# Performance work log

Hardware: AMD Instinct MI355X
Metric: run time of the kernel (lower is better)

The kernel has to match this reference:

```python
import jax, jax.numpy as jnp
import numpy as np

V, D, L, H, HD, S = 50257, 768, 8, 6, 128, 2048
BS = 128          # flex-attention BLOCK_SIZE
EOS = 50256       # document separator token
EPS = 1.1920929e-07  # torch F.rms_norm default eps (f32 machine eps)
ATTN_SCALE = 0.12


def rms(x):
    return x * jax.lax.rsqrt(jnp.mean(jnp.square(x), axis=-1, keepdims=True) + EPS)


def rope_tables(seq_len, hd):
    # modded-nanogpt rotary: hd//4 geometric freqs + hd//4 zero freqs, applied to half-split dims
    freqs = (1.0 / 1024.0) ** jnp.linspace(0.0, 1.0, hd // 4)
    freqs = jnp.concatenate([freqs, jnp.zeros(hd // 4, dtype=jnp.float32)])
    theta = jnp.arange(seq_len, dtype=jnp.float32)[:, None] * freqs[None, :]  # [S, hd//2]
    return jnp.cos(theta), jnp.sin(theta)


def rope(x, cos, sin):  # x: [B,S,H,hd]
    x1, x2 = jnp.split(x, 2, axis=-1)
    c = cos[None, :, None, :]
    s = sin[None, :, None, :]
    return jnp.concatenate([x1 * c + x2 * s, -x1 * s + x2 * c], axis=-1)


def build_token_mask(input_seq, w):
    # Reproduces BlockMask.from_kv_blocks semantics: per query-row keep the w-1 most
    # recent FULL blocks and min(n_partial, max(w - n_full, 1)) most recent PARTIAL
    # blocks; mask_mod (document-causal) applies inside partial blocks only.
    NB = S // BS
    docs = jnp.cumsum((input_seq == EOS).astype(jnp.int32))
    bi = jnp.arange(NB)
    dr = docs.reshape(NB, BS)
    dl, dh = dr[:, 0], dr[:, -1]
    m_any = (bi[:, None] >= bi[None, :]) & (dl[:, None] <= dh[None, :]) & (dh[:, None] >= dl[None, :])
    m_all = (bi[:, None] > bi[None, :]) & (dl[:, None] == dh[None, :]) & (dh[:, None] == dl[None, :])
    part = m_any & ~m_all
    nf = m_all.sum(-1)

    def keep_most_recent(m, kcount):  # keep kcount True entries with largest kv index
        r = jnp.cumsum(m[:, ::-1].astype(jnp.int32), axis=-1)[:, ::-1]
        return m & (r <= kcount[:, None])

    kf = keep_most_recent(m_all, jnp.minimum(nf, w - 1))
    kp = keep_most_recent(part, jnp.minimum(part.sum(-1), jnp.maximum(w - nf, 1)))
    tf = jnp.repeat(jnp.repeat(kf, BS, 0), BS, 1)   # [S,S]
    tp = jnp.repeat(jnp.repeat(kp, BS, 0), BS, 1)
    q = jnp.arange(S)
    tok = (q[:, None] >= q[None, :]) & (docs[:, None] == docs[None, :])
    return tf | (tp & tok)


def _forward(input_seq, sliding_window_num_blocks, target_seq, embed, ve_embeds,
             qkv_w, attn_proj_w, mlp_fc_w, mlp_proj_w, scalars):
    cos, sin = rope_tables(S, HD)
    long_m = build_token_mask(input_seq, sliding_window_num_blocks)
    short_m = build_token_mask(input_seq, sliding_window_num_blocks // 2)
    cycle = [long_m, short_m, short_m, short_m]
    masks = (cycle * ((L + 3) // 4))[:L - 1] + [long_m]

    ve_tok = ve_embeds[:, input_seq, :]  # [3,S,D]
    ve = [ve_tok[0], ve_tok[1], ve_tok[2]] + [None] * (L - 6) + [ve_tok[0], ve_tok[1], ve_tok[2]]

    skip_w = scalars[:L]
    lambdas = scalars[L:3 * L].reshape(L, 2)
    sa_lambdas = scalars[3 * L:5 * L].reshape(L, 2)

    stride = max(1, L // 4)
    skip_map = {}
    for m in range(3):
        i = L - 3 + m
        j = i - stride * (m + 1)
        if 0 <= j < i < L:
            skip_map[i] = j

    x = x0 = rms(embed[input_seq])[None]  # [1,S,D]
    skips = []
    for i in range(L):
        if i in skip_map:
            x = x + skip_w[skip_map[i]] * skips[skip_map[i]]
        lam, sal = lambdas[i], sa_lambdas[i]
        # Block: residual mix with x0, attn, mlp (modded-nanogpt style)
        x = lam[0] * x + lam[1] * x0
        xa = rms(x)
        qkv = (xa @ qkv_w[i].T).reshape(1, S, 3 * H, HD)
        q, k, v = jnp.split(qkv, 3, axis=2)
        q = rope(rms(q), cos, sin)
        k = rope(rms(k), cos, sin)
        if ve[i] is not None:
            v = sal[0] * v + sal[1] * ve[i].reshape(1, S, H, HD)
        else:
            v = sal[0] * v
        scores = jnp.einsum('bqhd,bkhd->bhqk', q, k) * ATTN_SCALE
        scores = jnp.where(masks[i][None, None], scores, -jnp.inf)
        y = jnp.einsum('bhqk,bkhd->bqhd', jax.nn.softmax(scores, axis=-1), v)
        x = x + y.reshape(1, S, H * HD) @ attn_proj_w[i].T
        h = jnp.square(jax.nn.relu(rms(x) @ mlp_fc_w[i].T))
        x = x + h @ mlp_proj_w[i].T
        skips.append(x)

    x = rms(x)
    logits = (x[0].astype(jnp.bfloat16) @ embed.T.astype(jnp.bfloat16)).astype(jnp.float32)
    cap = 15.0 * logits * jax.lax.rsqrt(jnp.square(logits) + 225.0)  # softcap
    lsm = jax.nn.log_softmax(cap, axis=-1)
    return -jnp.mean(lsm[jnp.arange(S), target_seq])


def setup_inputs() -> dict:
    key = jax.random.key(0)
    ks = jax.random.split(key, 9)
    input_seq = jax.random.randint(ks[0], (S,), 0, V)
    input_seq = input_seq.at[jnp.arange(0, S, 512)].set(EOS)  # inject doc boundaries
    target_seq = jax.random.randint(ks[1], (S,), 0, V)
    embed = jax.random.normal(ks[2], (V, D), jnp.float32)
    ve_embeds = jax.random.normal(ks[3], (3, V, D), jnp.float32)
    sd = 1.0 / np.sqrt(D)
    qkv_w = jax.random.normal(ks[4], (L, 3 * H * HD, D), jnp.float32) * sd
    attn_proj_w = jax.random.normal(ks[5], (L, D, H * HD), jnp.float32) * (1.0 / np.sqrt(H * HD))
    mlp_fc_w = jax.random.normal(ks[6], (L, 4 * D, D), jnp.float32) * sd
    mlp_proj_w = jax.random.normal(ks[7], (L, D, 4 * D), jnp.float32) * (1.0 / np.sqrt(4 * D))
    scalars = jnp.concatenate([
        jnp.ones(L), jnp.tile(jnp.array([1.0, 0.0]), L), jnp.tile(jnp.array([0.5, 0.5]), L)
    ]).astype(jnp.float32) + 0.02 * jax.random.normal(ks[8], (5 * L,), jnp.float32)
    return {"input_seq": input_seq, "sliding_window_num_blocks": 8, "target_seq": target_seq,
            "embed": embed, "ve_embeds": ve_embeds, "qkv_w": qkv_w, "attn_proj_w": attn_proj_w,
            "mlp_fc_w": mlp_fc_w, "mlp_proj_w": mlp_proj_w, "scalars": scalars}


def reference(input_seq, sliding_window_num_blocks, target_seq, embed, ve_embeds,
              qkv_w, attn_proj_w, mlp_fc_w, mlp_proj_w, scalars):
    return _forward(input_seq, sliding_window_num_blocks, target_seq, embed, ve_embeds,
                    qkv_w, attn_proj_w, mlp_fc_w, mlp_proj_w, scalars)
```

## Files before the change

### kernel.cpp

```cpp
#include <hip/hip_runtime.h>
#include <hip/hip_bf16.h>
#include <math.h>

#define NSEQ 2048
#define NDIM 768
#define NLAY 8
#define NHEAD 6
#define NHD 128
#define NVOC 50257
#define NBLK 16
#define BLKSZ 128
#define EOS_TOK 50256
#define EPSF 1.1920929e-07f
#define ASCALE 0.12f
#define NVT 393
#define CAPSH 15.f

#define GSWZ(r) (((r) ^ ((r) >> 2)) & 3)

using bf16x8 = __attribute__((ext_vector_type(8))) __bf16;
using bf16x4 = __attribute__((ext_vector_type(4))) __bf16;
using f32x4  = __attribute__((ext_vector_type(4))) float;

__device__ __forceinline__ __bf16 tobf(float x) {
  __hip_bfloat16 h = __float2bfloat16(x);
  return *reinterpret_cast<__bf16*>(&h);
}

__global__ __launch_bounds__(256) void cvt_bf16_kernel(const float* __restrict__ in, __bf16* __restrict__ out,
                                                       long n) {
  long i = ((long)blockIdx.x * blockDim.x + threadIdx.x) * 4;
  long stride = (long)gridDim.x * blockDim.x * 4;
  for (; i < n; i += stride) {
    float4 v = *(const float4*)(in + i);
    bf16x4 o;
    o[0] = tobf(v.x); o[1] = tobf(v.y); o[2] = tobf(v.z); o[3] = tobf(v.w);
    *(bf16x4*)(out + i) = o;
  }
}

__global__ __launch_bounds__(1024) void prep_kernel(const int* __restrict__ seq, const int* __restrict__ wptr,
                                                    int* __restrict__ docs, int* __restrict__ catL,
                                                    int* __restrict__ catS) {
  __shared__ int f[NSEQ];
  __shared__ int g[NSEQ];
  int tid = threadIdx.x;
  for (int i = tid; i < NSEQ; i += 1024) f[i] = (seq[i] == EOS_TOK) ? 1 : 0;
  __syncthreads();
  int* a = f; int* b = g;
  for (int off = 1; off < NSEQ; off <<= 1) {
    for (int i = tid; i < NSEQ; i += 1024) {
      int v = a[i];
      if (i >= off) v += a[i - off];
      b[i] = v;
    }
    __syncthreads();
    int* t = a; a = b; b = t;
  }
  for (int i = tid; i < NSEQ; i += 1024) docs[i] = a[i];
  __syncthreads();
  if (tid == 0) {
    int dl[NBLK], dh[NBLK];
    for (int bi = 0; bi < NBLK; ++bi) { dl[bi] = a[bi * BLKSZ]; dh[bi] = a[bi * BLKSZ + BLKSZ - 1]; }
    int W = *wptr;
    for (int pass = 0; pass < 2; ++pass) {
      int w = (pass == 0) ? W : (W / 2);
      int* cat = (pass == 0) ? catL : catS;
      for (int i = 0; i < NBLK; ++i) {
        int allr[NBLK], partr[NBLK];
        int nf = 0, np = 0;
        for (int j = 0; j < NBLK; ++j) {
          int any_ = (i >= j) && (dl[i] <= dh[j]) && (dh[i] >= dl[j]);
          int all_ = (i > j) && (dl[i] == dh[j]) && (dh[i] == dl[j]);
          allr[j] = all_; partr[j] = any_ && !all_;
          nf += all_; np += partr[j];
        }
        int kcf = min(nf, w - 1);
        int kcp = min(np, max(w - nf, 1));
        int cf = 0, cp = 0;
        for (int j = NBLK - 1; j >= 0; --j) {
          int cv = 0;
          if (allr[j]) { cf++; if (cf <= kcf) cv = 2; }
          if (partr[j]) { cp++; if (cp <= kcp) cv = 1; }
          cat[i * NBLK + j] = cv;
        }
      }
    }
  }
}

__global__ __launch_bounds__(256) void embed_rms_kernel(const int* __restrict__ seq, const float* __restrict__ embed,
                                                        float* __restrict__ x, float* __restrict__ x0) {
  int s = blockIdx.x;
  int tid = threadIdx.x;
  const float* row = embed + (size_t)seq[s] * NDIM;
  float v0 = row[tid], v1 = row[tid + 256], v2 = row[tid + 512];
  float ss = v0 * v0 + v1 * v1 + v2 * v2;
  __shared__ float red[256];
  red[tid] = ss; __syncthreads();
  for (int o = 128; o > 0; o >>= 1) { if (tid < o) red[tid] += red[tid + o]; __syncthreads(); }
  float sc = rsqrtf(red[0] / (float)NDIM + EPSF);
  size_t base = (size_t)s * NDIM;
  float o0 = v0 * sc, o1 = v1 * sc, o2 = v2 * sc;
  x[base + tid] = o0; x[base + tid + 256] = o1; x[base + tid + 512] = o2;
  x0[base + tid] = o0; x0[base + tid + 256] = o1; x0[base + tid + 512] = o2;
}

__global__ __launch_bounds__(256) void rmsbf_kernel(const float* __restrict__ x, __bf16* __restrict__ xb) {
  int s = blockIdx.x;
  int tid = threadIdx.x;
  size_t base = (size_t)s * NDIM;
  float v0 = x[base + tid], v1 = x[base + tid + 256], v2 = x[base + tid + 512];
  float ss = v0 * v0 + v1 * v1 + v2 * v2;
  __shared__ float red[256];
  red[tid] = ss; __syncthreads();
  for (int o = 128; o > 0; o >>= 1) { if (tid < o) red[tid] += red[tid + o]; __syncthreads(); }
  float sc = rsqrtf(red[0] / (float)NDIM + EPSF);
  xb[base + tid] = tobf(v0 * sc); xb[base + tid + 256] = tobf(v1 * sc); xb[base + tid + 512] = tobf(v2 * sc);
}

__global__ __launch_bounds__(256) void mixrms_kernel(float* __restrict__ x, const float* __restrict__ x0,
                                                     const float* __restrict__ skip, const float* __restrict__ scal,
                                                     int li, int sj, __bf16* __restrict__ xb) {
  float lam0 = scal[NLAY + 2 * li], lam1 = scal[NLAY + 2 * li + 1];
  float sw = (sj >= 0) ? scal[sj] : 0.f;
  int s = blockIdx.x;
  int tid = threadIdx.x;
  size_t base = (size_t)s * NDIM;
  float xv[3], ov[3], nv[3];
  xv[0] = x[base + tid]; xv[1] = x[base + tid + 256]; xv[2] = x[base + tid + 512];
  ov[0] = x0[base + tid]; ov[1] = x0[base + tid + 256]; ov[2] = x0[base + tid + 512];
  if (skip) {
    nv[0] = lam0 * (xv[0] + sw * skip[base + tid])       + lam1 * ov[0];
    nv[1] = lam0 * (xv[1] + sw * skip[base + tid + 256]) + lam1 * ov[1];
    nv[2] = lam0 * (xv[2] + sw * skip[base + tid + 512]) + lam1 * ov[2];
  } else {
    nv[0] = lam0 * xv[0] + lam1 * ov[0];
    nv[1] = lam0 * xv[1] + lam1 * ov[1];
    nv[2] = lam0 * xv[2] + lam1 * ov[2];
  }
  x[base + tid] = nv[0]; x[base + tid + 256] = nv[1]; x[base + tid + 512] = nv[2];
  float ss = nv[0] * nv[0] + nv[1] * nv[1] + nv[2] * nv[2];
  __shared__ float red[256];
  red[tid] = ss; __syncthreads();
  for (int o = 128; o > 0; o >>= 1) { if (tid < o) red[tid] += red[tid + o]; __syncthreads(); }
  float sc = rsqrtf(red[0] / (float)NDIM + EPSF);
  xb[base + tid] = tobf(nv[0] * sc); xb[base + tid + 256] = tobf(nv[1] * sc); xb[base + tid + 512] = tobf(nv[2] * sc);
}

template <int MODE>
__global__ __launch_bounds__(256) void gemm_mfma(const __bf16* __restrict__ A, const __bf16* __restrict__ B,
                                                 float* __restrict__ Cf, __bf16* __restrict__ Cb,
                                                 int N, int K) {
  __shared__ __bf16 As[2][128 * 32];
  __shared__ __bf16 Bs[2][128 * 32];
  int bm = blockIdx.x * 128, bn = blockIdx.y * 128;
  int tid = threadIdx.x;
  int w = tid >> 6, l = tid & 63;
  int wm = (w >> 1) * 64, wn = (w & 1) * 64;
  int c = l & 15, g = l >> 4;

  auto stage = [&](int buf, int k0) {
#pragma unroll
    for (int i = 0; i < 2; ++i) {
      int L = (w * 2 + i) * 64 + l;
      int row = L >> 2, gc = L & 3;
      int gs = gc ^ GSWZ(row);
      const __bf16* srcA = A + (size_t)(bm + row) * K + k0 + gs * 8;
      const __bf16* srcB = B + (size_t)(bn + row) * K + k0 + gs * 8;
      __builtin_amdgcn_global_load_lds(
          (const __attribute__((address_space(1))) void*)srcA,
          (__attribute__((address_space(3))) void*)&As[buf][(w * 2 + i) * 512], 16, 0, 0);
      __builtin_amdgcn_global_load_lds(
          (const __attribute__((address_space(1))) void*)srcB,
          (__attribute__((address_space(3))) void*)&Bs[buf][(w * 2 + i) * 512], 16, 0, 0);
    }
  };

  f32x4 acc[4][4] = {};
  stage(0, 0);
  __syncthreads();
  int nk = K >> 5;
  for (int kk = 0; kk < nk; ++kk) {
    int buf = kk & 1;
    if (kk + 1 < nk) stage(buf ^ 1, (kk + 1) * 32);
    bf16x8 af[4], bfr[4];
#pragma unroll
    for (int i = 0; i < 4; ++i) {
      int row = wm + i * 16 + c;
      af[i] = *(const bf16x8*)&As[buf][row * 32 + (g ^ GSWZ(row)) * 8];
    }
#pragma unroll
    for (int j = 0; j < 4; ++j) {
      int row = wn + j * 16 + c;
      bfr[j] = *(const bf16x8*)&Bs[buf][row * 32 + (g ^ GSWZ(row)) * 8];
    }
#pragma unroll
    for (int i = 0; i < 4; ++i)
#pragma unroll
      for (int j = 0; j < 4; ++j)
        acc[i][j] = __builtin_amdgcn_mfma_f32_16x16x32_bf16(af[i], bfr[j], acc[i][j], 0, 0, 0);
    __syncthreads();
  }
#pragma unroll
  for (int i = 0; i < 4; ++i)
#pragma unroll
    for (int j = 0; j < 4; ++j)
#pragma unroll
      for (int rr = 0; rr < 4; ++rr) {
        int row = bm + wm + i * 16 + g * 4 + rr;
        int col = bn + wn + j * 16 + c;
        size_t ci = (size_t)row * N + col;
        float z = acc[i][j][rr];
        if (MODE == 0) Cf[ci] = z;
        else if (MODE == 1) Cf[ci] += z;
        else { float r = fmaxf(z, 0.f); Cb[ci] = tobf(r * r); }
      }
}

template <int MODE>
__global__ __launch_bounds__(256) void gemm_mfma64(const __bf16* __restrict__ A, const __bf16* __restrict__ B,
                                                   float* __restrict__ Cf, __bf16* __restrict__ Cb,
                                                   int N, int K) {
  __shared__ __bf16 As[2][64 * 32];
  __shared__ __bf16 Bs[2][64 * 32];
  int bm = blockIdx.x * 64, bn = blockIdx.y * 64;
  int tid = threadIdx.x;
  int w = tid >> 6, l = tid & 63;
  int wm = (w >> 1) * 32, wn = (w & 1) * 32;
  int c = l & 15, g = l >> 4;

  auto stage = [&](int buf, int k0) {
    int L = w * 64 + l;
    int row = L >> 2, gc = L & 3;
    int gs = gc ^ GSWZ(row);
    const __bf16* srcA = A + (size_t)(bm + row) * K + k0 + gs * 8;
    const __bf16* srcB = B + (size_t)(bn + row) * K + k0 + gs * 8;
    __builtin_amdgcn_global_load_lds(
        (const __attribute__((address_space(1))) void*)srcA,
        (__attribute__((address_space(3))) void*)&As[buf][w * 512], 16, 0, 0);
    __builtin_amdgcn_global_load_lds(
        (const __attribute__((address_space(1))) void*)srcB,
        (__attribute__((address_space(3))) void*)&Bs[buf][w * 512], 16, 0, 0);
  };

  f32x4 acc[2][2] = {};
  stage(0, 0);
  __syncthreads();
  int nk = K >> 5;
  for (int kk = 0; kk < nk; ++kk) {
    int buf = kk & 1;
    if (kk + 1 < nk) stage(buf ^ 1, (kk + 1) * 32);
    bf16x8 af[2], bfr[2];
#pragma unroll
    for (int i = 0; i < 2; ++i) {
      int row = wm + i * 16 + c;
      af[i] = *(const bf16x8*)&As[buf][row * 32 + (g ^ GSWZ(row)) * 8];
    }
#pragma unroll
    for (int j = 0; j < 2; ++j) {
      int row = wn + j * 16 + c;
      bfr[j] = *(const bf16x8*)&Bs[buf][row * 32 + (g ^ GSWZ(row)) * 8];
    }
#pragma unroll
    for (int i = 0; i < 2; ++i)
#pragma unroll
      for (int j = 0; j < 2; ++j)
        acc[i][j] = __builtin_amdgcn_mfma_f32_16x16x32_bf16(af[i], bfr[j], acc[i][j], 0, 0, 0);
    __syncthreads();
  }
#pragma unroll
  for (int i = 0; i < 2; ++i)
#pragma unroll
    for (int j = 0; j < 2; ++j)
#pragma unroll
      for (int rr = 0; rr < 4; ++rr) {
        int row = bm + wm + i * 16 + g * 4 + rr;
        int col = bn + wn + j * 16 + c;
        size_t ci = (size_t)row * N + col;
        float z = acc[i][j][rr];
        if (MODE == 0) Cf[ci] = z;
        else if (MODE == 1) Cf[ci] += z;
        else { float r = fmaxf(z, 0.f); Cb[ci] = tobf(r * r); }
      }
}

__global__ __launch_bounds__(256) void qkv_post_kernel(const float* __restrict__ qkv, const float* __restrict__ vemb,
                                                       const int* __restrict__ seq, const float* __restrict__ scal,
                                                       int li, int ve_idx,
                                                       __bf16* __restrict__ qo, __bf16* __restrict__ ko,
                                                       __bf16* __restrict__ vo) {
  int p = blockIdx.x * 4 + (threadIdx.x >> 6);
  int l = threadIdx.x & 63;
  int h = p >> 11;
  int s = p & (NSEQ - 1);
  float sal0 = scal[3 * NLAY + 2 * li], sal1 = scal[3 * NLAY + 2 * li + 1];
  float fr = (l < 32) ? powf(1.0f / 1024.0f, (float)l * (1.0f / 31.0f)) : 0.f;
  float th = (float)s * fr;
  float cth = cosf(th), sth = sinf(th);
  size_t rb = (size_t)s * (3 * NHEAD * NHD) + h * NHD;
  float q0 = qkv[rb + l],                 q1 = qkv[rb + l + 64];
  float k0 = qkv[rb + NHEAD * NHD + l],   k1 = qkv[rb + NHEAD * NHD + l + 64];
  float v0 = qkv[rb + 2 * NHEAD * NHD + l], v1 = qkv[rb + 2 * NHEAD * NHD + l + 64];
  float ssq = q0 * q0 + q1 * q1;
  float ssk = k0 * k0 + k1 * k1;
#pragma unroll
  for (int o = 1; o < 64; o <<= 1) {
    ssq += __shfl_xor(ssq, o, 64);
    ssk += __shfl_xor(ssk, o, 64);
  }
  float scq = rsqrtf(ssq / (float)NHD + EPSF);
  float sck = rsqrtf(ssk / (float)NHD + EPSF);
  float qn0 = q0 * scq, qn1 = q1 * scq;
  float kn0 = k0 * sck, kn1 = k1 * sck;
  float oq0 = qn0 * cth + qn1 * sth, oq1 = -qn0 * sth + qn1 * cth;
  float ok0 = kn0 * cth + kn1 * sth, ok1 = -kn0 * sth + kn1 * cth;
  float ov0 = sal0 * v0, ov1 = sal0 * v1;
  if (ve_idx >= 0) {
    const float* ver = vemb + ((size_t)ve_idx * NVOC + seq[s]) * NDIM + h * NHD;
    ov0 += sal1 * ver[l];
    ov1 += sal1 * ver[l + 64];
  }
  size_t oo = ((size_t)h * NSEQ + s) * NHD;
  qo[oo + l] = tobf(oq0); qo[oo + l + 64] = tobf(oq1);
  ko[oo + l] = tobf(ok0); ko[oo + l + 64] = tobf(ok1);
  vo[oo + l] = tobf(ov0); vo[oo + l + 64] = tobf(ov1);
}

__global__ __launch_bounds__(256) void vtrans_kernel(const __bf16* __restrict__ v, __bf16* __restrict__ vt) {
  int st = blockIdx.x * 64, dt = blockIdx.y * 64, h = blockIdx.z;
  __shared__ __bf16 t[64][65];
  int tid = threadIdx.x;
  for (int e = tid; e < 4096; e += 256) {
    int s = e >> 6, d = e & 63;
    t[s][d] = v[((size_t)h * NSEQ + st + s) * NHD + dt + d];
  }
  __syncthreads();
  for (int e = tid; e < 512; e += 256) {
    int d = e >> 3, s0 = (e & 7) * 8;
    bf16x8 ov;
#pragma unroll
    for (int i = 0; i < 8; ++i) ov[i] = t[s0 + i][d];
    *(bf16x8*)(vt + ((size_t)h * NHD + dt + d) * NSEQ + st + s0) = ov;
  }
}

__global__ __launch_bounds__(256) void attn_mfma_kernel(const __bf16* __restrict__ qb, const __bf16* __restrict__ kb,
                                                        const __bf16* __restrict__ vt, const int* __restrict__ cat,
                                                        const int* __restrict__ docs, __bf16* __restrict__ y) {
  int qb32 = (int)gridDim.x - 1 - (int)blockIdx.x;
  int h = blockIdx.y;
  int tid = threadIdx.x;
  int wq = tid >> 6;
  int pr = wq >> 1;
  int sub = wq & 1;
  int l = tid & 63;
  int c = l & 15, g = l >> 4;
  int q0 = qb32 * 32 + sub * 16;
  int qB = qb32 >> 2;

  __shared__ __align__(16) char arena[65536];
  __bf16* Ks  = (__bf16*)arena;
  __bf16* Vts = (__bf16*)(arena + 32768);
  __shared__ __bf16 Ps[4][16 * 32];
  __shared__ int kvs[64];
  __shared__ int kvc[64];
  __shared__ int nact_s;

  if (tid == 0) {
    int n = 0;
    for (int kv = 0; kv <= qb32; ++kv) {
      int cc = cat[qB * NBLK + (kv >> 2)];
      if (cc) { kvs[n] = kv; kvc[n] = cc; ++n; }
    }
    nact_s = n;
  }

  bf16x8 qf[4];
#pragma unroll
  for (int ks = 0; ks < 4; ++ks)
    qf[ks] = *(const bf16x8*)(qb + ((size_t)h * NSEQ + q0 + c) * NHD + ks * 32 + g * 8);

  int qd[4];
#pragma unroll
  for (int rr = 0; rr < 4; ++rr) qd[rr] = docs[q0 + g * 4 + rr];

  float m[4], lden[4];
#pragma unroll
  for (int rr = 0; rr < 4; ++rr) { m[rr] = -INFINITY; lden[rr] = 0.f; }
  f32x4 oacc[8] = {};

  __syncthreads();
  int nact = nact_s;
  int nit = (nact + 1) >> 1;

  auto stage = [&](int ti, int bufi) {
    int kv = kvs[ti];
#pragma unroll
    for (int i = 0; i < 4; ++i) {
      int L = (sub * 4 + i) * 64 + l;
      int krow = L >> 4, gl = L & 15;
      int gs = gl ^ (krow & 7);
      const __bf16* srcK = kb + ((size_t)h * NSEQ + kv * 32 + krow) * NHD + gs * 8;
      __builtin_amdgcn_global_load_lds(
          (const __attribute__((address_space(1))) void*)srcK,
          (__attribute__((address_space(3))) void*)&Ks[(pr * 2 + bufi) * 4096 + (sub * 4 + i) * 512], 16, 0, 0);
      int drow = L >> 2, gk = L & 3;
      const __bf16* srcV = vt + ((size_t)h * NHD + drow) * NSEQ + kv * 32 + gk * 8;
      __builtin_amdgcn_global_load_lds(
          (const __attribute__((address_space(1))) void*)srcV,
          (__attribute__((address_space(3))) void*)&Vts[(pr * 2 + bufi) * 4096 + (sub * 4 + i) * 512], 16, 0, 0);
    }
  };

  if (pr < nact) stage(pr, 0);
  __syncthreads();

  for (int it = 0; it < nit; ++it) {
    int buf = it & 1;
    int tin = 2 * (it + 1) + pr;
    if (tin < nact) stage(tin, buf ^ 1);
    int ti = 2 * it + pr;
    if (ti < nact) {
      int kv = kvs[ti], cc = kvc[ti];
      int k0 = kv * 32;
      const __bf16* Kb = &Ks[(pr * 2 + buf) * 4096];
      const __bf16* Vb = &Vts[(pr * 2 + buf) * 4096];

      f32x4 sacc[2] = {};
#pragma unroll
      for (int ks = 0; ks < 4; ++ks) {
#pragma unroll
        for (int j = 0; j < 2; ++j) {
          int row = j * 16 + c;
          int gi = (ks * 4 + g) ^ (row & 7);
          bf16x8 kf = *(const bf16x8*)&Kb[row * 128 + gi * 8];
          sacc[j] = __builtin_amdgcn_mfma_f32_16x16x32_bf16(qf[ks], kf, sacc[j], 0, 0, 0);
        }
      }
      float sc[2][4];
      float bmax[4] = {-INFINITY, -INFINITY, -INFINITY, -INFINITY};
#pragma unroll
      for (int j = 0; j < 2; ++j) {
        int key = k0 + j * 16 + c;
        int kdj = docs[key];
#pragma unroll
        for (int rr = 0; rr < 4; ++rr) {
          int qrow = q0 + g * 4 + rr;
          bool ok = (cc == 2) || ((key <= qrow) && (kdj == qd[rr]));
          float z = ok ? sacc[j][rr] * ASCALE : -INFINITY;
          sc[j][rr] = z;
          bmax[rr] = fmaxf(bmax[rr], z);
        }
      }
#pragma unroll
      for (int rr = 0; rr < 4; ++rr) {
        bmax[rr] = fmaxf(bmax[rr], __shfl_xor(bmax[rr], 1, 64));
        bmax[rr] = fmaxf(bmax[rr], __shfl_xor(bmax[rr], 2, 64));
        bmax[rr] = fmaxf(bmax[rr], __shfl_xor(bmax[rr], 4, 64));
        bmax[rr] = fmaxf(bmax[rr], __shfl_xor(bmax[rr], 8, 64));
      }
      float corr[4], psum[4];
#pragma unroll
      for (int rr = 0; rr < 4; ++rr) {
        float mnew = fmaxf(m[rr], bmax[rr]);
        float msafe = (mnew == -INFINITY) ? 0.f : mnew;
        corr[rr] = __expf(m[rr] - msafe);
        float p0 = __expf(sc[0][rr] - msafe);
        float p1 = __expf(sc[1][rr] - msafe);
        sc[0][rr] = p0; sc[1][rr] = p1;
        psum[rr] = p0 + p1;
        m[rr] = mnew;
      }
#pragma unroll
      for (int rr = 0; rr < 4; ++rr) {
        psum[rr] += __shfl_xor(psum[rr], 1, 64);
        psum[rr] += __shfl_xor(psum[rr], 2, 64);
        psum[rr] += __shfl_xor(psum[rr], 4, 64);
        psum[rr] += __shfl_xor(psum[rr], 8, 64);
        lden[rr] = lden[rr] * corr[rr] + psum[rr];
      }
#pragma unroll
      for (int nt = 0; nt < 8; ++nt)
#pragma unroll
        for (int rr = 0; rr < 4; ++rr) oacc[nt][rr] *= corr[rr];
#pragma unroll
      for (int j = 0; j < 2; ++j)
#pragma unroll
        for (int rr = 0; rr < 4; ++rr)
          Ps[wq][(g * 4 + rr) * 32 + j * 16 + c] = tobf(sc[j][rr]);
      asm volatile("s_waitcnt lgkmcnt(0)" ::: "memory");
      bf16x8 pf = *(const bf16x8*)&Ps[wq][c * 32 + g * 8];
#pragma unroll
      for (int nt = 0; nt < 8; ++nt) {
        bf16x8 vf = *(const bf16x8*)&Vb[(nt * 16 + c) * 32 + g * 8];
        oacc[nt] = __builtin_amdgcn_mfma_f32_16x16x32_bf16(pf, vf, oacc[nt], 0, 0, 0);
      }
    }
    __syncthreads();
  }

  float* mrg = (float*)arena;
  if (pr == 1) {
    int base = (sub * 64 + l) * 40;
#pragma unroll
    for (int rr = 0; rr < 4; ++rr) { mrg[base + rr] = m[rr]; mrg[base + 4 + rr] = lden[rr]; }
#pragma unroll
    for (int nt = 0; nt < 8; ++nt)
#pragma unroll
      for (int rr = 0; rr < 4; ++rr) mrg[base + 8 + nt * 4 + rr] = oacc[nt][rr];
  }
  __syncthreads();
  if (pr == 0) {
    int base = (sub * 64 + l) * 40;
    float w0[4], w1[4], inv[4];
#pragma unroll
    for (int rr = 0; rr < 4; ++rr) {
      float m1v = mrg[base + rr];
      float l1v = mrg[base + 4 + rr];
      float M = fmaxf(m[rr], m1v);
      float msafe = (M == -INFINITY) ? 0.f : M;
      w0[rr] = __expf(m[rr] - msafe);
      w1[rr] = __expf(m1v - msafe);
      float L = lden[rr] * w0[rr] + l1v * w1[rr];
      inv[rr] = (L > 0.f) ? 1.f / L : 0.f;
    }
#pragma unroll
    for (int nt = 0; nt < 8; ++nt)
#pragma unroll
      for (int rr = 0; rr < 4; ++rr) {
        int qrow = q0 + g * 4 + rr;
        float o = oacc[nt][rr] * w0[rr] + mrg[base + 8 + nt * 4 + rr] * w1[rr];
        y[(size_t)qrow * NDIM + h * NHD + nt * 16 + c] = tobf(o * inv[rr]);
      }
  }
}

__global__ __launch_bounds__(256) void logits_gemm_kernel(const __bf16* __restrict__ xbf,
                                                          const __bf16* __restrict__ embed_bf,
                                                          const int* __restrict__ target,
                                                          float* __restrict__ part_l,
                                                          float* __restrict__ tcap) {
  __shared__ __bf16 As[2][128 * 32];
  __shared__ __bf16 Bs[2][128 * 32];
  __shared__ float rs2[2][128];
  int lid = (int)blockIdx.y * (int)gridDim.x + (int)blockIdx.x;
  int nid = (lid & 7) * 786 + (lid >> 3);
  int bm = (nid & 15) * 128;
  int vt = nid >> 4;
  int bn = vt * 128;
  int tid = threadIdx.x;
  int w = tid >> 6, l = tid & 63;
  int wm = (w >> 1) * 64, wn = (w & 1) * 64;
  int c = l & 15, g = l >> 4;

  auto stage = [&](int buf, int k0) {
#pragma unroll
    for (int i = 0; i < 2; ++i) {
      int L = (w * 2 + i) * 64 + l;
      int row = L >> 2, gc = L & 3;
      int gs = gc ^ GSWZ(row);
      int vrow = bn + row;
      if (vrow >= NVOC) vrow = NVOC - 1;
      const __bf16* srcA = xbf + (size_t)(bm + row) * NDIM + k0 + gs * 8;
      const __bf16* srcB = embed_bf + (size_t)vrow * NDIM + k0 + gs * 8;
      __builtin_amdgcn_global_load_lds(
          (const __attribute__((address_space(1))) void*)srcA,
          (__attribute__((address_space(3))) void*)&As[buf][(w * 2 + i) * 512], 16, 0, 0);
      __builtin_amdgcn_global_load_lds(
          (const __attribute__((address_space(1))) void*)srcB,
          (__attribute__((address_space(3))) void*)&Bs[buf][(w * 2 + i) * 512], 16, 0, 0);
    }
  };

  f32x4 acc[4][4] = {};
  stage(0, 0);
  __syncthreads();
  const int nk = NDIM / 32;
  for (int kk = 0; kk < nk; ++kk) {
    int buf = kk & 1;
    if (kk + 1 < nk) stage(buf ^ 1, (kk + 1) * 32);
    bf16x8 af[4], bfr[4];
#pragma unroll
    for (int i = 0; i < 4; ++i) {
      int row = wm + i * 16 + c;
      af[i] = *(const bf16x8*)&As[buf][row * 32 + (g ^ GSWZ(row)) * 8];
    }
#pragma unroll
    for (int j = 0; j < 4; ++j) {
      int row = wn + j * 16 + c;
      bfr[j] = *(const bf16x8*)&Bs[buf][row * 32 + (g ^ GSWZ(row)) * 8];
    }
#pragma unroll
    for (int i = 0; i < 4; ++i)
#pragma unroll
      for (int j = 0; j < 4; ++j)
        acc[i][j] = __builtin_amdgcn_mfma_f32_16x16x32_bf16(af[i], bfr[j], acc[i][j], 0, 0, 0);
    __syncthreads();
  }

#pragma unroll
  for (int i = 0; i < 4; ++i) {
#pragma unroll
    for (int rr = 0; rr < 4; ++rr) {
      int rowl = wm + i * 16 + g * 4 + rr;
      int tg = target[bm + rowl];
      float ts = 0.f;
#pragma unroll
      for (int j = 0; j < 4; ++j) {
        int vv = bn + wn + j * 16 + c;
        bool okv = vv < NVOC;
        float z = acc[i][j][rr];
        float cp = 15.f * z * rsqrtf(z * z + 225.f);
        ts += okv ? __expf(cp - CAPSH) : 0.f;
        if (okv && vv == tg) tcap[bm + rowl] = cp;
      }
      ts += __shfl_xor(ts, 1, 64);
      ts += __shfl_xor(ts, 2, 64);
      ts += __shfl_xor(ts, 4, 64);
      ts += __shfl_xor(ts, 8, 64);
      if (c == 0) rs2[w & 1][rowl] = ts;
    }
  }
  __syncthreads();
  if (tid < 128) {
    part_l[(size_t)vt * NSEQ + bm + tid] = rs2[0][tid] + rs2[1][tid];
  }
}

__global__ __launch_bounds__(256) void lossrow_kernel(const float* __restrict__ part_l,
                                                      const float* __restrict__ tcap, float* __restrict__ lr) {
  int row = blockIdx.x * 256 + threadIdx.x;
  float L = 0.f;
  for (int cc = 0; cc < NVT; ++cc) L += part_l[(size_t)cc * NSEQ + row];
  lr[row] = (CAPSH + logf(L)) - tcap[row];
}

__global__ __launch_bounds__(256) void loss2_kernel(const float* __restrict__ lr, float* __restrict__ out) {
  int tid = threadIdx.x;
  float sum = 0.f;
  for (int t = tid; t < NSEQ; t += 256) sum += lr[t];
  __shared__ float red[256];
  red[tid] = sum; __syncthreads();
  for (int o = 128; o > 0; o >>= 1) { if (tid < o) red[tid] += red[tid + o]; __syncthreads(); }
  if (tid == 0) out[0] = red[0] / (float)NSEQ;
}

extern "C" void kernel_launch(void* const* d_in, const int* in_sizes, int n_in,
                              void* d_out, int out_size, void* d_ws, size_t ws_size,
                              hipStream_t stream) {
  const int* seq   = (const int*)d_in[0];
  const int* wnb   = (const int*)d_in[1];
  const int* tgt   = (const int*)d_in[2];
  const float* embed = (const float*)d_in[3];
  const float* vemb  = (const float*)d_in[4];
  const float* qkvw  = (const float*)d_in[5];
  const float* aprj  = (const float*)d_in[6];
  const float* fcw   = (const float*)d_in[7];
  const float* prjw  = (const float*)d_in[8];
  const float* scal  = (const float*)d_in[9];
  float* out = (float*)d_out;

  char* w = (char*)d_ws;
  auto alloc = [&](size_t bytes) {
    char* p = w;
    w += (bytes + 255) & ~(size_t)255;
    return p;
  };
  int* docs = (int*)alloc(NSEQ * 4);
  int* catL = (int*)alloc(NBLK * NBLK * 4);
  int* catS = (int*)alloc(NBLK * NBLK * 4);
  float* x    = (float*)alloc((size_t)NSEQ * NDIM * 4);
  float* x0   = (float*)alloc((size_t)NSEQ * NDIM * 4);
  float* sk1  = (float*)alloc((size_t)NSEQ * NDIM * 4);
  float* sk2  = (float*)alloc((size_t)NSEQ * NDIM * 4);
  float* sk3  = (float*)alloc((size_t)NSEQ * NDIM * 4);
  float* qkvb = (float*)alloc((size_t)NSEQ * 3 * NHEAD * NHD * 4);
  __bf16* qbf2 = (__bf16*)alloc((size_t)NHEAD * NSEQ * NHD * 2);
  __bf16* kbf2 = (__bf16*)alloc((size_t)NHEAD * NSEQ * NHD * 2);
  __bf16* vbf2 = (__bf16*)alloc((size_t)NHEAD * NSEQ * NHD * 2);
  __bf16* vtbf = (__bf16*)alloc((size_t)NHEAD * NHD * NSEQ * 2);
  __bf16* xabf = (__bf16*)alloc((size_t)NSEQ * NDIM * 2);
  __bf16* ybf  = (__bf16*)alloc((size_t)NSEQ * NDIM * 2);
  __bf16* hbf  = (__bf16*)alloc((size_t)NSEQ * 4 * NDIM * 2);
  __bf16* xbf  = (__bf16*)alloc((size_t)NSEQ * NDIM * 2);
  float* pl   = (float*)alloc((size_t)NVT * NSEQ * 4);
  float* tc   = (float*)alloc((size_t)NSEQ * 4);
  float* lrow = (float*)alloc((size_t)NSEQ * 4);
  __bf16* embbf = (__bf16*)alloc((size_t)NVOC * NDIM * 2);
  __bf16* qkvwbf = (__bf16*)alloc((size_t)NLAY * 3 * NHEAD * NHD * NDIM * 2);
  __bf16* aprjbf = (__bf16*)alloc((size_t)NLAY * NDIM * NDIM * 2);
  __bf16* fcwbf  = (__bf16*)alloc((size_t)NLAY * 4 * NDIM * NDIM * 2);
  __bf16* prjwbf = (__bf16*)alloc((size_t)NLAY * NDIM * 4 * NDIM * 2);
  float* skips[4] = {nullptr, sk1, sk2, sk3};

  cvt_bf16_kernel<<<2048, 256, 0, stream>>>(embed, embbf, (long)NVOC * NDIM);
  cvt_bf16_kernel<<<2048, 256, 0, stream>>>(qkvw, qkvwbf, (long)NLAY * 3 * NHEAD * NHD * NDIM);
  cvt_bf16_kernel<<<2048, 256, 0, stream>>>(aprj, aprjbf, (long)NLAY * NDIM * NDIM);
  cvt_bf16_kernel<<<2048, 256, 0, stream>>>(fcw, fcwbf, (long)NLAY * 4 * NDIM * NDIM);
  cvt_bf16_kernel<<<2048, 256, 0, stream>>>(prjw, prjwbf, (long)NLAY * NDIM * 4 * NDIM);

  prep_kernel<<<1, 1024, 0, stream>>>(seq, wnb, docs, catL, catS);
  embed_rms_kernel<<<NSEQ, 256, 0, stream>>>(seq, embed, x, x0);

  const int velist[NLAY]   = {0, 1, 2, -1, -1, 0, 1, 2};
  const int skipj[NLAY]    = {-1, -1, -1, -1, -1, 3, 2, 1};
  const int maskLong[NLAY] = {1, 0, 0, 0, 1, 0, 0, 1};

  for (int i = 0; i < NLAY; ++i) {
    mixrms_kernel<<<NSEQ, 256, 0, stream>>>(x, x0, skipj[i] >= 0 ? skips[skipj[i]] : nullptr, scal, i, skipj[i], xabf);
    gemm_mfma64<0><<<dim3(NSEQ / 64, (3 * NHEAD * NHD) / 64), 256, 0, stream>>>(
        xabf, qkvwbf + (size_t)i * 3 * NHEAD * NHD * NDIM, qkvb, nullptr, 3 * NHEAD * NHD, NDIM);
    qkv_post_kernel<<<NHEAD * NSEQ / 4, 256, 0, stream>>>(qkvb, vemb, seq, scal, i, velist[i], qbf2, kbf2, vbf2);
    vtrans_kernel<<<dim3(NSEQ / 64, NHD / 64, NHEAD), 256, 0, stream>>>(vbf2, vtbf);
    attn_mfma_kernel<<<dim3(NSEQ / 32, NHEAD), 256, 0, stream>>>(qbf2, kbf2, vtbf, maskLong[i] ? catL : catS, docs, ybf);
    gemm_mfma64<1><<<dim3(NSEQ / 64, NDIM / 64), 256, 0, stream>>>(
        ybf, aprjbf + (size_t)i * NDIM * NDIM, x, nullptr, NDIM, NDIM);
    rmsbf_kernel<<<NSEQ, 256, 0, stream>>>(x, xabf);
    gemm_mfma64<2><<<dim3(NSEQ / 64, (4 * NDIM) / 64), 256, 0, stream>>>(
        xabf, fcwbf + (size_t)i * 4 * NDIM * NDIM, nullptr, hbf, 4 * NDIM, NDIM);
    gemm_mfma64<1><<<dim3(NSEQ / 64, NDIM / 64), 256, 0, stream>>>(
        hbf, prjwbf + (size_t)i * NDIM * 4 * NDIM, x, nullptr, NDIM, 4 * NDIM);
    if (i >= 1 && i <= 3) {
      hipMemcpyAsync(skips[i], x, (size_t)NSEQ * NDIM * 4, hipMemcpyDeviceToDevice, stream);
    }
  }

  rmsbf_kernel<<<NSEQ, 256, 0, stream>>>(x, xbf);
  logits_gemm_kernel<<<dim3(NSEQ / 128, NVT), 256, 0, stream>>>(xbf, embbf, tgt, pl, tc);
  lossrow_kernel<<<NSEQ / 256, 256, 0, stream>>>(pl, tc, lrow);
  loss2_kernel<<<1, 256, 0, stream>>>(lrow, out);
}
```

Baseline: 1.694 ms.

## Use BK=64 GEMM tiles, bf16 QKV output, and fuse skip copy into epilogue

The 64x64 GEMM now stages 64-wide K slices with an 8-way XOR swizzle, which halves the number of k-iterations and barriers. The QKV projection writes bf16 instead of f32, and qkv_post reads bf16, cutting that intermediate's traffic in half but adding one extra rounding step. The skip-connection device copy after layers 1-3 is replaced by a new epilogue mode that writes the residual to both x and the skip buffer. The unused 128x128 GEMM variant is removed.

```diff
diff --git a/kernel.cpp b/kernel.cpp
--- a/kernel.cpp
+++ b/kernel.cpp
@@ -25,6 +25,10 @@
 __device__ __forceinline__ __bf16 tobf(float x) {
   __hip_bfloat16 h = __float2bfloat16(x);
   return *reinterpret_cast<__bf16*>(&h);
+}
+__device__ __forceinline__ float frombf(__bf16 x) {
+  __hip_bfloat16 h = *reinterpret_cast<__hip_bfloat16*>(&x);
+  return __bfloat162float(h);
 }
 
 __global__ __launch_bounds__(256) void cvt_bf16_kernel(const float* __restrict__ in, __bf16* __restrict__ out,
@@ -149,23 +153,23 @@
 }
 
 template <int MODE>
-__global__ __launch_bounds__(256) void gemm_mfma(const __bf16* __restrict__ A, const __bf16* __restrict__ B,
-                                                 float* __restrict__ Cf, __bf16* __restrict__ Cb,
-                                                 int N, int K) {
-  __shared__ __bf16 As[2][128 * 32];
-  __shared__ __bf16 Bs[2][128 * 32];
-  int bm = blockIdx.x * 128, bn = blockIdx.y * 128;
+__global__ __launch_bounds__(256) void gemm_mfma64(const __bf16* __restrict__ A, const __bf16* __restrict__ B,
+                                                   float* __restrict__ Cf, __bf16* __restrict__ Cb,
+                                                   float* __restrict__ Sk, int N, int K) {
+  __shared__ __bf16 As[2][64 * 64];
+  __shared__ __bf16 Bs[2][64 * 64];
+  int bm = blockIdx.x * 64, bn = blockIdx.y * 64;
   int tid = threadIdx.x;
   int w = tid >> 6, l = tid & 63;
-  int wm = (w >> 1) * 64, wn = (w & 1) * 64;
+  int wm = (w >> 1) * 32, wn = (w & 1) * 32;
   int c = l & 15, g = l >> 4;
 
   auto stage = [&](int buf, int k0) {
 #pragma unroll
     for (int i = 0; i < 2; ++i) {
       int L = (w * 2 + i) * 64 + l;
-      int row = L >> 2, gc = L & 3;
-      int gs = gc ^ GSWZ(row);
+      int row = L >> 3, gl = L & 7;
+      int gs = gl ^ (row & 7);
       const __bf16* srcA = A + (size_t)(bm + row) * K + k0 + gs * 8;
       const __bf16* srcB = B + (size_t)(bn + row) * K + k0 + gs * 8;
       __builtin_amdgcn_global_load_lds(
@@ -177,35 +181,38 @@
     }
   };
 
-  f32x4 acc[4][4] = {};
+  f32x4 acc[2][2] = {};
   stage(0, 0);
   __syncthreads();
-  int nk = K >> 5;
+  int nk = K >> 6;
   for (int kk = 0; kk < nk; ++kk) {
     int buf = kk & 1;
-    if (kk + 1 < nk) stage(buf ^ 1, (kk + 1) * 32);
-    bf16x8 af[4], bfr[4];
-#pragma unroll
-    for (int i = 0; i < 4; ++i) {
-      int row = wm + i * 16 + c;
-      af[i] = *(const bf16x8*)&As[buf][row * 32 + (g ^ GSWZ(row)) * 8];
-    }
-#pragma unroll
-    for (int j = 0; j < 4; ++j) {
-      int row = wn + j * 16 + c;
-      bfr[j] = *(const bf16x8*)&Bs[buf][row * 32 + (g ^ GSWZ(row)) * 8];
-    }
-#pragma unroll
-    for (int i = 0; i < 4; ++i)
-#pragma unroll
-      for (int j = 0; j < 4; ++j)
-        acc[i][j] = __builtin_amdgcn_mfma_f32_16x16x32_bf16(af[i], bfr[j], acc[i][j], 0, 0, 0);
+    if (kk + 1 < nk) stage(buf ^ 1, (kk + 1) * 64);
+#pragma unroll
+    for (int ks = 0; ks < 2; ++ks) {
+      bf16x8 af[2], bfr[2];
+#pragma unroll
+      for (int i = 0; i < 2; ++i) {
+        int row = wm + i * 16 + c;
+        af[i] = *(const bf16x8*)&As[buf][row * 64 + ((ks * 4 + g) ^ (row & 7)) * 8];
+      }
+#pragma unroll
+      for (int j = 0; j < 2; ++j) {
+        int row = wn + j * 16 + c;
+        bfr[j] = *(const bf16x8*)&Bs[buf][row * 64 + ((ks * 4 + g) ^ (row & 7)) * 8];
+      }
+#pragma unroll
+      for (int i = 0; i < 2; ++i)
+#pragma unroll
+        for (int j = 0; j < 2; ++j)
+          acc[i][j] = __builtin_amdgcn_mfma_f32_16x16x32_bf16(af[i], bfr[j], acc[i][j], 0, 0, 0);
+    }
     __syncthreads();
   }
 #pragma unroll
-  for (int i = 0; i < 4; ++i)
-#pragma unroll
-    for (int j = 0; j < 4; ++j)
+  for (int i = 0; i < 2; ++i)
+#pragma unroll
+    for (int j = 0; j < 2; ++j)
 #pragma unroll
       for (int rr = 0; rr < 4; ++rr) {
         int row = bm + wm + i * 16 + g * 4 + rr;
@@ -214,78 +221,13 @@
         float z = acc[i][j][rr];
         if (MODE == 0) Cf[ci] = z;
         else if (MODE == 1) Cf[ci] += z;
-        else { float r = fmaxf(z, 0.f); Cb[ci] = tobf(r * r); }
-      }
-}
-
-template <int MODE>
-__global__ __launch_bounds__(256) void gemm_mfma64(const __bf16* __restrict__ A, const __bf16* __restrict__ B,
-                                                   float* __restrict__ Cf, __bf16* __restrict__ Cb,
-                                                   int N, int K) {
-  __shared__ __bf16 As[2][64 * 32];
-  __shared__ __bf16 Bs[2][64 * 32];
-  int bm = blockIdx.x * 64, bn = blockIdx.y * 64;
-  int tid = threadIdx.x;
-  int w = tid >> 6, l = tid & 63;
-  int wm = (w >> 1) * 32, wn = (w & 1) * 32;
-  int c = l & 15, g = l >> 4;
-
-  auto stage = [&](int buf, int k0) {
-    int L = w * 64 + l;
-    int row = L >> 2, gc = L & 3;
-    int gs = gc ^ GSWZ(row);
-    const __bf16* srcA = A + (size_t)(bm + row) * K + k0 + gs * 8;
-    const __bf16* srcB = B + (size_t)(bn + row) * K + k0 + gs * 8;
-    __builtin_amdgcn_global_load_lds(
-        (const __attribute__((address_space(1))) void*)srcA,
-        (__attribute__((address_space(3))) void*)&As[buf][w * 512], 16, 0, 0);
-    __builtin_amdgcn_global_load_lds(
-        (const __attribute__((address_space(1))) void*)srcB,
-        (__attribute__((address_space(3))) void*)&Bs[buf][w * 512], 16, 0, 0);
-  };
-
-  f32x4 acc[2][2] = {};
-  stage(0, 0);
-  __syncthreads();
-  int nk = K >> 5;
-  for (int kk = 0; kk < nk; ++kk) {
-    int buf = kk & 1;
-    if (kk + 1 < nk) stage(buf ^ 1, (kk + 1) * 32);
-    bf16x8 af[2], bfr[2];
-#pragma unroll
-    for (int i = 0; i < 2; ++i) {
-      int row = wm + i * 16 + c;
-      af[i] = *(const bf16x8*)&As[buf][row * 32 + (g ^ GSWZ(row)) * 8];
-    }
-#pragma unroll
-    for (int j = 0; j < 2; ++j) {
-      int row = wn + j * 16 + c;
-      bfr[j] = *(const bf16x8*)&Bs[buf][row * 32 + (g ^ GSWZ(row)) * 8];
-    }
-#pragma unroll
-    for (int i = 0; i < 2; ++i)
-#pragma unroll
-      for (int j = 0; j < 2; ++j)
-        acc[i][j] = __builtin_amdgcn_mfma_f32_16x16x32_bf16(af[i], bfr[j], acc[i][j], 0, 0, 0);
-    __syncthreads();
-  }
-#pragma unroll
-  for (int i = 0; i < 2; ++i)
-#pragma unroll
-    for (int j = 0; j < 2; ++j)
-#pragma unroll
-      for (int rr = 0; rr < 4; ++rr) {
-        int row = bm + wm + i * 16 + g * 4 + rr;
-        int col = bn + wn + j * 16 + c;
-        size_t ci = (size_t)row * N + col;
-        float z = acc[i][j][rr];
-        if (MODE == 0) Cf[ci] = z;
-        else if (MODE == 1) Cf[ci] += z;
-        else { float r = fmaxf(z, 0.f); Cb[ci] = tobf(r * r); }
-      }
-}
-
-__global__ __launch_bounds__(256) void qkv_post_kernel(const float* __restrict__ qkv, const float* __restrict__ vemb,
+        else if (MODE == 2) { float r = fmaxf(z, 0.f); Cb[ci] = tobf(r * r); }
+        else if (MODE == 3) Cb[ci] = tobf(z);
+        else { float s = Cf[ci] + z; Cf[ci] = s; Sk[ci] = s; }
+      }
+}
+
+__global__ __launch_bounds__(256) void qkv_post_kernel(const __bf16* __restrict__ qkv, const float* __restrict__ vemb,
                                                        const int* __restrict__ seq, const float* __restrict__ scal,
                                                        int li, int ve_idx,
                                                        __bf16* __restrict__ qo, __bf16* __restrict__ ko,
@@ -299,9 +241,9 @@
   float th = (float)s * fr;
   float cth = cosf(th), sth = sinf(th);
   size_t rb = (size_t)s * (3 * NHEAD * NHD) + h * NHD;
-  float q0 = qkv[rb + l],                 q1 = qkv[rb + l + 64];
-  float k0 = qkv[rb + NHEAD * NHD + l],   k1 = qkv[rb + NHEAD * NHD + l + 64];
-  float v0 = qkv[rb + 2 * NHEAD * NHD + l], v1 = qkv[rb + 2 * NHEAD * NHD + l + 64];
+  float q0 = frombf(qkv[rb + l]),                 q1 = frombf(qkv[rb + l + 64]);
+  float k0 = frombf(qkv[rb + NHEAD * NHD + l]),   k1 = frombf(qkv[rb + NHEAD * NHD + l + 64]);
+  float v0 = frombf(qkv[rb + 2 * NHEAD * NHD + l]), v1 = frombf(qkv[rb + 2 * NHEAD * NHD + l + 64]);
   float ssq = q0 * q0 + q1 * q1;
   float ssk = k0 * k0 + k1 * k1;
 #pragma unroll
@@ -675,7 +617,7 @@
   float* sk1  = (float*)alloc((size_t)NSEQ * NDIM * 4);
   float* sk2  = (float*)alloc((size_t)NSEQ * NDIM * 4);
   float* sk3  = (float*)alloc((size_t)NSEQ * NDIM * 4);
-  float* qkvb = (float*)alloc((size_t)NSEQ * 3 * NHEAD * NHD * 4);
+  __bf16* qkvbf = (__bf16*)alloc((size_t)NSEQ * 3 * NHEAD * NHD * 2);
   __bf16* qbf2 = (__bf16*)alloc((size_t)NHEAD * NSEQ * NHD * 2);
   __bf16* kbf2 = (__bf16*)alloc((size_t)NHEAD * NSEQ * NHD * 2);
   __bf16* vbf2 = (__bf16*)alloc((size_t)NHEAD * NSEQ * NHD * 2);
@@ -709,20 +651,22 @@
 
   for (int i = 0; i < NLAY; ++i) {
     mixrms_kernel<<<NSEQ, 256, 0, stream>>>(x, x0, skipj[i] >= 0 ? skips[skipj[i]] : nullptr, scal, i, skipj[i], xabf);
-    gemm_mfma64<0><<<dim3(NSEQ / 64, (3 * NHEAD * NHD) / 64), 256, 0, stream>>>(
-        xabf, qkvwbf + (size_t)i * 3 * NHEAD * NHD * NDIM, qkvb, nullptr, 3 * NHEAD * NHD, NDIM);
-    qkv_post_kernel<<<NHEAD * NSEQ / 4, 256, 0, stream>>>(qkvb, vemb, seq, scal, i, velist[i], qbf2, kbf2, vbf2);
+    gemm_mfma64<3><<<dim3(NSEQ / 64, (3 * NHEAD * NHD) / 64), 256, 0, stream>>>(
+        xabf, qkvwbf + (size_t)i * 3 * NHEAD * NHD * NDIM, nullptr, qkvbf, nullptr, 3 * NHEAD * NHD, NDIM);
+    qkv_post_kernel<<<NHEAD * NSEQ / 4, 256, 0, stream>>>(qkvbf, vemb, seq, scal, i, velist[i], qbf2, kbf2, vbf2);
     vtrans_kernel<<<dim3(NSEQ / 64, NHD / 64, NHEAD), 256, 0, stream>>>(vbf2, vtbf);
     attn_mfma_kernel<<<dim3(NSEQ / 32, NHEAD), 256, 0, stream>>>(qbf2, kbf2, vtbf, maskLong[i] ? catL : catS, docs, ybf);
     gemm_mfma64<1><<<dim3(NSEQ / 64, NDIM / 64), 256, 0, stream>>>(
-        ybf, aprjbf + (size_t)i * NDIM * NDIM, x, nullptr, NDIM, NDIM);
+        ybf, aprjbf + (size_t)i * NDIM * NDIM, x, nullptr, nullptr, NDIM, NDIM);
     rmsbf_kernel<<<NSEQ, 256, 0, stream>>>(x, xabf);
     gemm_mfma64<2><<<dim3(NSEQ / 64, (4 * NDIM) / 64), 256, 0, stream>>>(
-        xabf, fcwbf + (size_t)i * 4 * NDIM * NDIM, nullptr, hbf, 4 * NDIM, NDIM);
-    gemm_mfma64<1><<<dim3(NSEQ / 64, NDIM / 64), 256, 0, stream>>>(
-        hbf, prjwbf + (size_t)i * NDIM * 4 * NDIM, x, nullptr, NDIM, 4 * NDIM);
+        xabf, fcwbf + (size_t)i * 4 * NDIM * NDIM, nullptr, hbf, nullptr, 4 * NDIM, NDIM);
     if (i >= 1 && i <= 3) {
-      hipMemcpyAsync(skips[i], x, (size_t)NSEQ * NDIM * 4, hipMemcpyDeviceToDevice, stream);
+      gemm_mfma64<4><<<dim3(NSEQ / 64, NDIM / 64), 256, 0, stream>>>(
+          hbf, prjwbf + (size_t)i * NDIM * 4 * NDIM, x, nullptr, skips[i], NDIM, 4 * NDIM);
+    } else {
+      gemm_mfma64<1><<<dim3(NSEQ / 64, NDIM / 64), 256, 0, stream>>>(
+          hbf, prjwbf + (size_t)i * NDIM * 4 * NDIM, x, nullptr, nullptr, NDIM, 4 * NDIM);
     }
   }
 
```

After: 1.663 ms. Within noise of the previous version (-1.8%).
